# Performance work log

Hardware: AMD Instinct MI355X
Metric: run time of the kernel (lower is better)

Reference implementation:

```python
import jax, jax.numpy as jnp
import numpy as np

N, E = 50000, 800000          # nodes, directed edges (before self-loops)
IN, H, C = 128, 8, 32         # in_feats, heads, per-head channels (= h_feats)
G = 64                        # graphs in batch
NEG_SLOPE = 0.2               # PyG GATConv default leaky_relu slope


def setup_inputs() -> dict:
    key = jax.random.key(0)
    ks = jax.random.split(key, 8)
    x = jax.random.normal(ks[0], (N, IN), jnp.float32)
    edge_index = jax.random.randint(ks[1], (2, E), 0, N)
    batch = jnp.sort(jax.random.randint(ks[2], (N,), 0, G))
    W = jax.random.normal(ks[3], (IN, H * C), jnp.float32) * 0.05
    att_src = jax.random.normal(ks[4], (H, C), jnp.float32) * 0.1
    att_dst = jax.random.normal(ks[5], (H, C), jnp.float32) * 0.1
    bias = jnp.zeros((C,), jnp.float32)
    lin_w = jax.random.normal(ks[6], (C, 2), jnp.float32) * 0.1
    lin_b = jnp.zeros((2,), jnp.float32)
    return dict(x=x, edge_index=edge_index, batch=batch, W=W,
                att_src=att_src, att_dst=att_dst, bias=bias,
                lin_w=lin_w, lin_b=lin_b)


def gat_conv(x, edge_index, W, att_src, att_dst, bias):
    # PyG GATConv, heads=H, concat=False, add_self_loops=True
    n = x.shape[0]
    h = (x @ W).reshape(n, H, C)                      # [N,H,C]
    loops = jnp.arange(n, dtype=edge_index.dtype)
    src = jnp.concatenate([edge_index[0], loops])     # [E+N]
    dst = jnp.concatenate([edge_index[1], loops])
    a_src = jnp.einsum('nhc,hc->nh', h, att_src)      # [N,H]
    a_dst = jnp.einsum('nhc,hc->nh', h, att_dst)
    e = jax.nn.leaky_relu(a_src[src] + a_dst[dst], NEG_SLOPE)  # [E+N,H]
    # segment softmax over edges sharing the same destination node
    m = jax.ops.segment_max(e, dst, num_segments=n)
    m = jnp.where(jnp.isfinite(m), m, 0.0)            # guard isolated nodes
    w = jnp.exp(e - m[dst])
    denom = jax.ops.segment_sum(w, dst, num_segments=n)
    alpha = w / (denom[dst] + 1e-16)                  # [E+N,H]
    out = jax.ops.segment_sum(h[src] * alpha[:, :, None], dst, num_segments=n)  # [N,H,C]
    return out.mean(axis=1) + bias                    # concat=False -> head mean


def reference(x, edge_index, batch, W, att_src, att_dst, bias, lin_w, lin_b):
    hid = jax.nn.relu(gat_conv(x, edge_index, W, att_src, att_dst, bias))  # [N,C]
    sums = jax.ops.segment_sum(hid, batch, num_segments=G)                  # [G,C]
    cnt = jax.ops.segment_sum(jnp.ones((hid.shape[0],), hid.dtype), batch,
                              num_segments=G)
    pooled = sums / jnp.maximum(cnt, 1.0)[:, None]    # global_mean_pool
    # Dropout(0.5) is identity in eval mode
    x_t = pooled @ lin_w + lin_b                      # [G,2]
    return (x_t, pooled)
```

## Files before the change

### kernel.cpp

```cpp
#include <hip/hip_runtime.h>
#include <hip/hip_bf16.h>

#define N_NODES 50000
#define E_EDGES 800000
#define IN_F 128
#define H_HEADS 8
#define C_CH 32
#define HC 256
#define G_GRAPHS 64
#define NEG_SLOPE 0.2f
#define NCHUNK 49

__device__ __forceinline__ unsigned short f2bf(float f) {
    unsigned u = __float_as_uint(f);
    u += 0x7fffu + ((u >> 16) & 1u);
    return (unsigned short)(u >> 16);
}

__global__ __launch_bounds__(256) void k_gemm(const float* __restrict__ x,
        const float* __restrict__ W, const float* __restrict__ att_src,
        const float* __restrict__ att_dst, unsigned short* __restrict__ hb,
        float* __restrict__ a_src, float* __restrict__ a_dst) {
    __shared__ float xs[8 * IN_F];
    const int n0 = blockIdx.x * 8;
    const int tid = threadIdx.x;
    ((float4*)xs)[tid] = ((const float4*)(x + (size_t)n0 * IN_F))[tid];
    __syncthreads();

    const int j = tid;
    float acc[8];
    #pragma unroll
    for (int r = 0; r < 8; ++r) acc[r] = 0.f;

    const float4* xs4 = (const float4*)xs;
    for (int k4 = 0; k4 < IN_F / 4; ++k4) {
        const float w0 = W[(k4 * 4 + 0) * HC + j];
        const float w1 = W[(k4 * 4 + 1) * HC + j];
        const float w2 = W[(k4 * 4 + 2) * HC + j];
        const float w3 = W[(k4 * 4 + 3) * HC + j];
        #pragma unroll
        for (int r = 0; r < 8; ++r) {
            float4 xv = xs4[r * (IN_F / 4) + k4];
            acc[r] += xv.x * w0 + xv.y * w1 + xv.z * w2 + xv.w * w3;
        }
    }

    const float asv = att_src[j], adv = att_dst[j];
    const int hh = j >> 5;
    #pragma unroll
    for (int r = 0; r < 8; ++r) {
        hb[(size_t)(n0 + r) * HC + j] = f2bf(acc[r]);
        float s = acc[r] * asv, d = acc[r] * adv;
        #pragma unroll
        for (int off = 16; off; off >>= 1) {
            s += __shfl_xor(s, off, 64);
            d += __shfl_xor(d, off, 64);
        }
        if ((tid & 31) == 0) {
            a_src[(n0 + r) * H_HEADS + hh] = s;
            a_dst[(n0 + r) * H_HEADS + hh] = d;
        }
    }
}

__global__ __launch_bounds__(256) void k_hist(const int* __restrict__ ei,
        int* __restrict__ deg) {
    int i = blockIdx.x * 256 + threadIdx.x;
    if (i < E_EDGES) atomicAdd(deg + ei[E_EDGES + i], 1);
}

__global__ __launch_bounds__(256) void k_chunksum(const int* __restrict__ deg,
        int* __restrict__ chunk) {
    __shared__ int ws4[4];
    const int tid = threadIdx.x, lane = tid & 63, wid = tid >> 6;
    const int base = blockIdx.x * 1024 + tid * 4;
    int s = 0;
    #pragma unroll
    for (int u = 0; u < 4; ++u) {
        int i = base + u;
        if (i < N_NODES) s += deg[i];
    }
    #pragma unroll
    for (int o = 32; o; o >>= 1) s += __shfl_xor(s, o, 64);
    if (lane == 0) ws4[wid] = s;
    __syncthreads();
    if (tid == 0) chunk[blockIdx.x] = ws4[0] + ws4[1] + ws4[2] + ws4[3];
}

__global__ __launch_bounds__(64) void k_chunkscan(const int* __restrict__ chunk,
        int* __restrict__ chunkoff) {
    int t = threadIdx.x;
    int v = (t < NCHUNK) ? chunk[t] : 0;
    int s = v;
    #pragma unroll
    for (int d = 1; d < 64; d <<= 1) {
        int u = __shfl_up(s, d, 64);
        if (t >= d) s += u;
    }
    if (t < NCHUNK) chunkoff[t] = s - v;
}

__global__ __launch_bounds__(1024) void k_localscan(const int* __restrict__ deg,
        const int* __restrict__ chunkoff, int* __restrict__ off,
        int* __restrict__ cursor) {
    __shared__ int wsum[16];
    const int tid = threadIdx.x, lane = tid & 63, wid = tid >> 6;
    const int i = blockIdx.x * 1024 + tid;
    int v = (i < N_NODES) ? deg[i] : 0;
    int s = v;
    #pragma unroll
    for (int d = 1; d < 64; d <<= 1) {
        int t = __shfl_up(s, d, 64);
        if (lane >= d) s += t;
    }
    if (lane == 63) wsum[wid] = s;
    __syncthreads();
    if (wid == 0 && lane < 16) {
        int t = wsum[lane];
        #pragma unroll
        for (int d = 1; d < 16; d <<= 1) {
            int u = __shfl_up(t, d, 64);
            if (lane >= d) t += u;
        }
        wsum[lane] = t;
    }
    __syncthreads();
    int wpre = wid ? wsum[wid - 1] : 0;
    if (i < N_NODES) {
        int excl = chunkoff[blockIdx.x] + wpre + s - v;
        off[i] = excl;
        cursor[i] = excl;
    }
    if (blockIdx.x == NCHUNK - 1 && tid == 0) off[N_NODES] = E_EDGES;
}

__global__ __launch_bounds__(256) void k_scatter(const int* __restrict__ ei,
        int* __restrict__ cursor, int* __restrict__ csr_src) {
    int i = blockIdx.x * 256 + threadIdx.x;
    if (i >= E_EDGES) return;
    int dst = ei[E_EDGES + i];
    int p = atomicAdd(cursor + dst, 1);
    csr_src[p] = ei[i];
}

__device__ __forceinline__ void bf4_unpack(uint2 q, float& x0, float& x1,
                                           float& x2, float& x3) {
    x0 = __uint_as_float(q.x << 16);
    x1 = __uint_as_float(q.x & 0xffff0000u);
    x2 = __uint_as_float(q.y << 16);
    x3 = __uint_as_float(q.y & 0xffff0000u);
}

__global__ __launch_bounds__(256) void k_node(const unsigned short* __restrict__ hb,
        const float* __restrict__ a_src, const float* __restrict__ a_dst,
        const int* __restrict__ off, const int* __restrict__ csr_src,
        const int* __restrict__ batch, const float* __restrict__ bias,
        float* __restrict__ pool, float* __restrict__ cnt) {
    const int wave = threadIdx.x >> 6, lane = threadIdx.x & 63;
    const int n = blockIdx.x * 4 + wave;
    if (n >= N_NODES) return;
    const int hh = lane >> 3;
    const int beg = off[n], end = off[n + 1];
    const float adst = a_dst[n * H_HEADS + hh];

    float denom = 0.f;
    float ax = 0.f, ay = 0.f, az = 0.f, aw = 0.f;
    {
        float e = a_src[n * H_HEADS + hh] + adst;
        e = e > 0.f ? e : NEG_SLOPE * e;
        float w = __expf(e);
        denom += w;
        uint2 q = ((const uint2*)(hb + (size_t)n * HC))[lane];
        float x0, x1, x2, x3; bf4_unpack(q, x0, x1, x2, x3);
        ax += w * x0; ay += w * x1; az += w * x2; aw += w * x3;
    }

    int k = beg;
    for (; k + 7 < end; k += 8) {
        int s[8];
        #pragma unroll
        for (int u = 0; u < 8; ++u) s[u] = csr_src[k + u];
        uint2 q[8];
        #pragma unroll
        for (int u = 0; u < 8; ++u)
            q[u] = ((const uint2*)(hb + (size_t)s[u] * HC))[lane];
        float e[8];
        #pragma unroll
        for (int u = 0; u < 8; ++u) e[u] = a_src[s[u] * H_HEADS + hh] + adst;
        #pragma unroll
        for (int u = 0; u < 8; ++u) {
            float ee = e[u] > 0.f ? e[u] : NEG_SLOPE * e[u];
            float w = __expf(ee);
            denom += w;
            float x0, x1, x2, x3; bf4_unpack(q[u], x0, x1, x2, x3);
            ax += w * x0; ay += w * x1; az += w * x2; aw += w * x3;
        }
    }
    for (; k < end; ++k) {
        int src = csr_src[k];
        float e = a_src[src * H_HEADS + hh] + adst;
        e = e > 0.f ? e : NEG_SLOPE * e;
        float w = __expf(e);
        denom += w;
        uint2 q = ((const uint2*)(hb + (size_t)src * HC))[lane];
        float x0, x1, x2, x3; bf4_unpack(q, x0, x1, x2, x3);
        ax += w * x0; ay += w * x1; az += w * x2; aw += w * x3;
    }

    const float inv = 1.f / (denom + 1e-16f);
    float rx = ax * inv, ry = ay * inv, rz = az * inv, rw = aw * inv;
    #pragma unroll
    for (int o = 8; o < 64; o <<= 1) {
        rx += __shfl_xor(rx, o, 64);
        ry += __shfl_xor(ry, o, 64);
        rz += __shfl_xor(rz, o, 64);
        rw += __shfl_xor(rw, o, 64);
    }
    if (lane < 8) {
        const int c0 = lane * 4;
        const int g = batch[n];
        float o0 = fmaxf(rx * 0.125f + bias[c0 + 0], 0.f);
        float o1 = fmaxf(ry * 0.125f + bias[c0 + 1], 0.f);
        float o2 = fmaxf(rz * 0.125f + bias[c0 + 2], 0.f);
        float o3 = fmaxf(rw * 0.125f + bias[c0 + 3], 0.f);
        float* pg = pool + g * C_CH + c0;
        atomicAdd(pg + 0, o0); atomicAdd(pg + 1, o1);
        atomicAdd(pg + 2, o2); atomicAdd(pg + 3, o3);
        if (lane == 0) atomicAdd(cnt + g, 1.f);
    }
}

__global__ __launch_bounds__(256) void k_final(const float* __restrict__ pool,
        const float* __restrict__ cnt, const float* __restrict__ lin_w,
        const float* __restrict__ lin_b, float* __restrict__ out) {
    __shared__ float pd[G_GRAPHS * C_CH];
    int t = threadIdx.x;
    for (int i = t; i < G_GRAPHS * C_CH; i += 256) {
        int g = i >> 5;
        float p = pool[i] / fmaxf(cnt[g], 1.f);
        pd[i] = p;
        out[G_GRAPHS * 2 + i] = p;
    }
    __syncthreads();
    if (t < G_GRAPHS * 2) {
        int g = t >> 1, o = t & 1;
        float s = lin_b[o];
        #pragma unroll
        for (int c = 0; c < C_CH; ++c) s += pd[g * C_CH + c] * lin_w[c * 2 + o];
        out[t] = s;
    }
}

extern "C" void kernel_launch(void* const* d_in, const int* in_sizes, int n_in,
                              void* d_out, int out_size, void* d_ws, size_t ws_size,
                              hipStream_t stream) {
    const float* x       = (const float*)d_in[0];
    const int*   ei      = (const int*)d_in[1];
    const int*   batch   = (const int*)d_in[2];
    const float* W       = (const float*)d_in[3];
    const float* att_src = (const float*)d_in[4];
    const float* att_dst = (const float*)d_in[5];
    const float* bias    = (const float*)d_in[6];
    const float* lin_w   = (const float*)d_in[7];
    const float* lin_b   = (const float*)d_in[8];

    char* ws = (char*)d_ws;
    unsigned short* hb   = (unsigned short*)(ws);
    float* a_src   = (float*)(ws + 25600000);
    float* a_dst   = (float*)(ws + 27200000);
    int*   deg     = (int*)  (ws + 28800000);
    int*   chunk   = (int*)  (ws + 29000000);
    int*   off     = (int*)  (ws + 29000256);
    int*   cursor  = (int*)  (ws + 29200512);
    int*   csr_src = (int*)  (ws + 29400512);
    float* pool    = (float*)(ws + 32600512);
    float* cnt     = (float*)(ws + 32608704);
    int*   chunkoff= (int*)  (ws + 32608960);

    hipMemsetAsync(deg, 0, 200000, stream);
    hipMemsetAsync(pool, 0, 8192 + 256, stream);

    k_gemm<<<N_NODES / 8, 256, 0, stream>>>(x, W, att_src, att_dst, hb, a_src, a_dst);
    k_hist<<<(E_EDGES + 255) / 256, 256, 0, stream>>>(ei, deg);
    k_chunksum<<<NCHUNK, 256, 0, stream>>>(deg, chunk);
    k_chunkscan<<<1, 64, 0, stream>>>(chunk, chunkoff);
    k_localscan<<<NCHUNK, 1024, 0, stream>>>(deg, chunkoff, off, cursor);
    k_scatter<<<(E_EDGES + 255) / 256, 256, 0, stream>>>(ei, cursor, csr_src);
    k_node<<<(N_NODES + 3) / 4, 256, 0, stream>>>(
        hb, a_src, a_dst, off, csr_src, batch, bias, pool, cnt);
    k_final<<<1, 256, 0, stream>>>(pool, cnt, lin_w, lin_b, (float*)d_out);
}
```

Before: 730.9 us.

## Process two edges per wave with 16-byte gathers and software-pipelined loads

The node aggregation kernel now splits each 64-lane wave into two halves. Each half handles a different edge and loads a 512-byte bf16 row with uint4 (16-byte) loads instead of uint2. The main loop double-buffers batches of four gathers so the next batch's loads are in flight while the current one is accumulated. The halves are merged with a cross-half shuffle, and the reduction across heads and the pooling atomics are adjusted to 8 channels per lane. The aim is wider memory transactions and more memory-level parallelism, at the cost of more registers and some extra odd-count tail handling.

```diff
diff --git a/kernel.cpp b/kernel.cpp
--- a/kernel.cpp
+++ b/kernel.cpp
@@ -143,12 +143,15 @@
     csr_src[p] = ei[i];
 }
 
-__device__ __forceinline__ void bf4_unpack(uint2 q, float& x0, float& x1,
-                                           float& x2, float& x3) {
-    x0 = __uint_as_float(q.x << 16);
-    x1 = __uint_as_float(q.x & 0xffff0000u);
-    x2 = __uint_as_float(q.y << 16);
-    x3 = __uint_as_float(q.y & 0xffff0000u);
+__device__ __forceinline__ void accum8w(float* acc, uint4 q, float w) {
+    acc[0] += w * __uint_as_float(q.x << 16);
+    acc[1] += w * __uint_as_float(q.x & 0xffff0000u);
+    acc[2] += w * __uint_as_float(q.y << 16);
+    acc[3] += w * __uint_as_float(q.y & 0xffff0000u);
+    acc[4] += w * __uint_as_float(q.z << 16);
+    acc[5] += w * __uint_as_float(q.z & 0xffff0000u);
+    acc[6] += w * __uint_as_float(q.w << 16);
+    acc[7] += w * __uint_as_float(q.w & 0xffff0000u);
 }
 
 __global__ __launch_bounds__(256) void k_node(const unsigned short* __restrict__ hb,
@@ -159,73 +162,102 @@
     const int wave = threadIdx.x >> 6, lane = threadIdx.x & 63;
     const int n = blockIdx.x * 4 + wave;
     if (n >= N_NODES) return;
-    const int hh = lane >> 3;
+    const int half = lane >> 5;
+    const int l32 = lane & 31;
+    const int hh = l32 >> 2;
     const int beg = off[n], end = off[n + 1];
     const float adst = a_dst[n * H_HEADS + hh];
 
+    float acc[8] = {0.f, 0.f, 0.f, 0.f, 0.f, 0.f, 0.f, 0.f};
     float denom = 0.f;
-    float ax = 0.f, ay = 0.f, az = 0.f, aw = 0.f;
+
     {
         float e = a_src[n * H_HEADS + hh] + adst;
         e = e > 0.f ? e : NEG_SLOPE * e;
-        float w = __expf(e);
+        float w = half ? 0.f : __expf(e);
+        uint4 q = ((const uint4*)(hb + (size_t)n * HC))[l32];
         denom += w;
-        uint2 q = ((const uint2*)(hb + (size_t)n * HC))[lane];
-        float x0, x1, x2, x3; bf4_unpack(q, x0, x1, x2, x3);
-        ax += w * x0; ay += w * x1; az += w * x2; aw += w * x3;
-    }
-
-    int k = beg;
-    for (; k + 7 < end; k += 8) {
-        int s[8];
-        #pragma unroll
-        for (int u = 0; u < 8; ++u) s[u] = csr_src[k + u];
-        uint2 q[8];
-        #pragma unroll
-        for (int u = 0; u < 8; ++u)
-            q[u] = ((const uint2*)(hb + (size_t)s[u] * HC))[lane];
-        float e[8];
-        #pragma unroll
-        for (int u = 0; u < 8; ++u) e[u] = a_src[s[u] * H_HEADS + hh] + adst;
-        #pragma unroll
-        for (int u = 0; u < 8; ++u) {
-            float ee = e[u] > 0.f ? e[u] : NEG_SLOPE * e[u];
-            float w = __expf(ee);
+        accum8w(acc, q, w);
+    }
+
+    auto issue = [&](int kk, uint4* q, float* ea) {
+        #pragma unroll
+        for (int u = 0; u < 4; ++u) {
+            int s0 = csr_src[kk + 2 * u];
+            int s1 = csr_src[kk + 2 * u + 1];
+            int s = half ? s1 : s0;
+            q[u] = ((const uint4*)(hb + (size_t)s * HC))[l32];
+            ea[u] = a_src[s * H_HEADS + hh];
+        }
+    };
+    auto consume = [&](const uint4* q, const float* ea) {
+        #pragma unroll
+        for (int u = 0; u < 4; ++u) {
+            float e = ea[u] + adst;
+            e = e > 0.f ? e : NEG_SLOPE * e;
+            float w = __expf(e);
             denom += w;
-            float x0, x1, x2, x3; bf4_unpack(q[u], x0, x1, x2, x3);
-            ax += w * x0; ay += w * x1; az += w * x2; aw += w * x3;
-        }
-    }
-    for (; k < end; ++k) {
-        int src = csr_src[k];
-        float e = a_src[src * H_HEADS + hh] + adst;
+            accum8w(acc, q[u], w);
+        }
+    };
+
+    const int nfull = (end - beg) & ~7;
+    const int nb = nfull >> 3;
+    uint4 qA[4], qB[4];
+    float eA[4], eB[4];
+    if (nb > 0) {
+        issue(beg, qA, eA);
+        for (int b = 1; b < nb; ++b) {
+            if (b & 1) { issue(beg + 8 * b, qB, eB); consume(qA, eA); }
+            else       { issue(beg + 8 * b, qA, eA); consume(qB, eB); }
+        }
+        if (nb & 1) consume(qA, eA); else consume(qB, eB);
+    }
+
+    int k = beg + nfull;
+    for (; k + 1 < end; k += 2) {
+        int s0 = csr_src[k], s1 = csr_src[k + 1];
+        int s = half ? s1 : s0;
+        uint4 q = ((const uint4*)(hb + (size_t)s * HC))[l32];
+        float e = a_src[s * H_HEADS + hh] + adst;
         e = e > 0.f ? e : NEG_SLOPE * e;
         float w = __expf(e);
         denom += w;
-        uint2 q = ((const uint2*)(hb + (size_t)src * HC))[lane];
-        float x0, x1, x2, x3; bf4_unpack(q, x0, x1, x2, x3);
-        ax += w * x0; ay += w * x1; az += w * x2; aw += w * x3;
-    }
-
-    const float inv = 1.f / (denom + 1e-16f);
-    float rx = ax * inv, ry = ay * inv, rz = az * inv, rw = aw * inv;
-    #pragma unroll
-    for (int o = 8; o < 64; o <<= 1) {
-        rx += __shfl_xor(rx, o, 64);
-        ry += __shfl_xor(ry, o, 64);
-        rz += __shfl_xor(rz, o, 64);
-        rw += __shfl_xor(rw, o, 64);
-    }
-    if (lane < 8) {
-        const int c0 = lane * 4;
+        accum8w(acc, q, w);
+    }
+    if (k < end) {
+        int s = csr_src[k];
+        uint4 q = ((const uint4*)(hb + (size_t)s * HC))[l32];
+        float e = a_src[s * H_HEADS + hh] + adst;
+        e = e > 0.f ? e : NEG_SLOPE * e;
+        float w = half ? 0.f : __expf(e);
+        denom += w;
+        accum8w(acc, q, w);
+    }
+
+    #pragma unroll
+    for (int j = 0; j < 8; ++j) acc[j] += __shfl_xor(acc[j], 32, 64);
+    denom += __shfl_xor(denom, 32, 64);
+
+    const float inv = 0.125f / (denom + 1e-16f);
+    float r[8];
+    #pragma unroll
+    for (int j = 0; j < 8; ++j) r[j] = acc[j] * inv;
+    #pragma unroll
+    for (int o = 4; o <= 16; o <<= 1) {
+        #pragma unroll
+        for (int j = 0; j < 8; ++j) r[j] += __shfl_xor(r[j], o, 64);
+    }
+    if (lane < 4) {
         const int g = batch[n];
-        float o0 = fmaxf(rx * 0.125f + bias[c0 + 0], 0.f);
-        float o1 = fmaxf(ry * 0.125f + bias[c0 + 1], 0.f);
-        float o2 = fmaxf(rz * 0.125f + bias[c0 + 2], 0.f);
-        float o3 = fmaxf(rw * 0.125f + bias[c0 + 3], 0.f);
+        const int c0 = lane * 8;
         float* pg = pool + g * C_CH + c0;
-        atomicAdd(pg + 0, o0); atomicAdd(pg + 1, o1);
-        atomicAdd(pg + 2, o2); atomicAdd(pg + 3, o3);
+        #pragma unroll
+        for (int j = 0; j < 8; ++j) {
+            float o = r[j] + bias[c0 + j];
+            o = o > 0.f ? o : 0.f;
+            atomicAdd(pg + j, o);
+        }
         if (lane == 0) atomicAdd(cnt + g, 1.f);
     }
 }
```

Result: slower. 778.6 us (+6.5%).

## Switch node-parallel aggregation to edge-parallel with segmented atomic accumulation

Applied to the files above, without the earlier changes.

Replaces the per-destination-node wave loop with an edge-parallel kernel. Each wave handles 8 consecutive CSR-sorted edges, merges runs that share a destination, and atomically adds the weighted features and denominators into a float accumulator of size N×256. A self-loop kernel initialises the accumulator and a finalize kernel normalises, averages heads, applies ReLU and pools. This aims to remove load imbalance from varying in-degrees, at the cost of writing and reading a large fp32 accumulator, many float atomics, and an extra csr_dst array.

```diff
diff --git a/kernel.cpp b/kernel.cpp
--- a/kernel.cpp
+++ b/kernel.cpp
@@ -101,8 +101,7 @@
 }
 
 __global__ __launch_bounds__(1024) void k_localscan(const int* __restrict__ deg,
-        const int* __restrict__ chunkoff, int* __restrict__ off,
-        int* __restrict__ cursor) {
+        const int* __restrict__ chunkoff, int* __restrict__ cursor) {
     __shared__ int wsum[16];
     const int tid = threadIdx.x, lane = tid & 63, wid = tid >> 6;
     const int i = blockIdx.x * 1024 + tid;
@@ -126,21 +125,18 @@
     }
     __syncthreads();
     int wpre = wid ? wsum[wid - 1] : 0;
-    if (i < N_NODES) {
-        int excl = chunkoff[blockIdx.x] + wpre + s - v;
-        off[i] = excl;
-        cursor[i] = excl;
-    }
-    if (blockIdx.x == NCHUNK - 1 && tid == 0) off[N_NODES] = E_EDGES;
+    if (i < N_NODES) cursor[i] = chunkoff[blockIdx.x] + wpre + s - v;
 }
 
 __global__ __launch_bounds__(256) void k_scatter(const int* __restrict__ ei,
-        int* __restrict__ cursor, int* __restrict__ csr_src) {
+        int* __restrict__ cursor, int* __restrict__ csr_src,
+        int* __restrict__ csr_dst) {
     int i = blockIdx.x * 256 + threadIdx.x;
     if (i >= E_EDGES) return;
     int dst = ei[E_EDGES + i];
     int p = atomicAdd(cursor + dst, 1);
     csr_src[p] = ei[i];
+    csr_dst[p] = dst;
 }
 
 __device__ __forceinline__ void bf4_unpack(uint2 q, float& x0, float& x1,
@@ -151,83 +147,83 @@
     x3 = __uint_as_float(q.y & 0xffff0000u);
 }
 
-__global__ __launch_bounds__(256) void k_node(const unsigned short* __restrict__ hb,
+__global__ __launch_bounds__(256) void k_selfloop(const unsigned short* __restrict__ hb,
         const float* __restrict__ a_src, const float* __restrict__ a_dst,
-        const int* __restrict__ off, const int* __restrict__ csr_src,
-        const int* __restrict__ batch, const float* __restrict__ bias,
-        float* __restrict__ pool, float* __restrict__ cnt) {
+        float* __restrict__ outacc, float* __restrict__ den) {
     const int wave = threadIdx.x >> 6, lane = threadIdx.x & 63;
     const int n = blockIdx.x * 4 + wave;
     if (n >= N_NODES) return;
     const int hh = lane >> 3;
-    const int beg = off[n], end = off[n + 1];
-    const float adst = a_dst[n * H_HEADS + hh];
-
-    float denom = 0.f;
-    float ax = 0.f, ay = 0.f, az = 0.f, aw = 0.f;
-    {
-        float e = a_src[n * H_HEADS + hh] + adst;
+    float e = a_src[n * H_HEADS + hh] + a_dst[n * H_HEADS + hh];
+    e = e > 0.f ? e : NEG_SLOPE * e;
+    float w = __expf(e);
+    uint2 q = ((const uint2*)(hb + (size_t)n * HC))[lane];
+    float x0, x1, x2, x3; bf4_unpack(q, x0, x1, x2, x3);
+    float* oa = outacc + (size_t)n * HC + lane * 4;
+    oa[0] = w * x0; oa[1] = w * x1; oa[2] = w * x2; oa[3] = w * x3;
+    if ((lane & 7) == 0) den[n * H_HEADS + hh] = w;
+}
+
+__global__ __launch_bounds__(256) void k_edge(const unsigned short* __restrict__ hb,
+        const float* __restrict__ a_src, const float* __restrict__ a_dst,
+        const int* __restrict__ csr_src, const int* __restrict__ csr_dst,
+        float* __restrict__ outacc, float* __restrict__ den) {
+    const int wid = blockIdx.x * 4 + (threadIdx.x >> 6);
+    const int lane = threadIdx.x & 63;
+    const int kb = wid * 8;
+    if (kb >= E_EDGES) return;
+    const int hh = lane >> 3;
+
+    int s[8], d[8];
+    #pragma unroll
+    for (int u = 0; u < 8; ++u) { s[u] = csr_src[kb + u]; d[u] = csr_dst[kb + u]; }
+    uint2 q[8];
+    #pragma unroll
+    for (int u = 0; u < 8; ++u)
+        q[u] = ((const uint2*)(hb + (size_t)s[u] * HC))[lane];
+    float w[8];
+    #pragma unroll
+    for (int u = 0; u < 8; ++u) {
+        float e = a_src[s[u] * H_HEADS + hh] + a_dst[d[u] * H_HEADS + hh];
         e = e > 0.f ? e : NEG_SLOPE * e;
-        float w = __expf(e);
-        denom += w;
-        uint2 q = ((const uint2*)(hb + (size_t)n * HC))[lane];
-        float x0, x1, x2, x3; bf4_unpack(q, x0, x1, x2, x3);
-        ax += w * x0; ay += w * x1; az += w * x2; aw += w * x3;
-    }
-
-    int k = beg;
-    for (; k + 7 < end; k += 8) {
-        int s[8];
-        #pragma unroll
-        for (int u = 0; u < 8; ++u) s[u] = csr_src[k + u];
-        uint2 q[8];
-        #pragma unroll
-        for (int u = 0; u < 8; ++u)
-            q[u] = ((const uint2*)(hb + (size_t)s[u] * HC))[lane];
-        float e[8];
-        #pragma unroll
-        for (int u = 0; u < 8; ++u) e[u] = a_src[s[u] * H_HEADS + hh] + adst;
-        #pragma unroll
-        for (int u = 0; u < 8; ++u) {
-            float ee = e[u] > 0.f ? e[u] : NEG_SLOPE * e[u];
-            float w = __expf(ee);
-            denom += w;
-            float x0, x1, x2, x3; bf4_unpack(q[u], x0, x1, x2, x3);
-            ax += w * x0; ay += w * x1; az += w * x2; aw += w * x3;
-        }
-    }
-    for (; k < end; ++k) {
-        int src = csr_src[k];
-        float e = a_src[src * H_HEADS + hh] + adst;
-        e = e > 0.f ? e : NEG_SLOPE * e;
-        float w = __expf(e);
-        denom += w;
-        uint2 q = ((const uint2*)(hb + (size_t)src * HC))[lane];
-        float x0, x1, x2, x3; bf4_unpack(q, x0, x1, x2, x3);
-        ax += w * x0; ay += w * x1; az += w * x2; aw += w * x3;
-    }
-
-    const float inv = 1.f / (denom + 1e-16f);
-    float rx = ax * inv, ry = ay * inv, rz = az * inv, rw = aw * inv;
-    #pragma unroll
-    for (int o = 8; o < 64; o <<= 1) {
-        rx += __shfl_xor(rx, o, 64);
-        ry += __shfl_xor(ry, o, 64);
-        rz += __shfl_xor(rz, o, 64);
-        rw += __shfl_xor(rw, o, 64);
-    }
-    if (lane < 8) {
-        const int c0 = lane * 4;
-        const int g = batch[n];
-        float o0 = fmaxf(rx * 0.125f + bias[c0 + 0], 0.f);
-        float o1 = fmaxf(ry * 0.125f + bias[c0 + 1], 0.f);
-        float o2 = fmaxf(rz * 0.125f + bias[c0 + 2], 0.f);
-        float o3 = fmaxf(rw * 0.125f + bias[c0 + 3], 0.f);
-        float* pg = pool + g * C_CH + c0;
-        atomicAdd(pg + 0, o0); atomicAdd(pg + 1, o1);
-        atomicAdd(pg + 2, o2); atomicAdd(pg + 3, o3);
-        if (lane == 0) atomicAdd(cnt + g, 1.f);
-    }
+        w[u] = __expf(e);
+    }
+
+    float a0 = 0.f, a1 = 0.f, a2 = 0.f, a3 = 0.f, dn = 0.f;
+    #pragma unroll
+    for (int u = 0; u < 8; ++u) {
+        float x0, x1, x2, x3; bf4_unpack(q[u], x0, x1, x2, x3);
+        a0 += w[u] * x0; a1 += w[u] * x1;
+        a2 += w[u] * x2; a3 += w[u] * x3;
+        dn += w[u];
+        bool fl = (u == 7) ? true : (d[u + 1] != d[u]);
+        if (fl) {
+            float* oa = outacc + (size_t)d[u] * HC + lane * 4;
+            atomicAdd(oa + 0, a0); atomicAdd(oa + 1, a1);
+            atomicAdd(oa + 2, a2); atomicAdd(oa + 3, a3);
+            if ((lane & 7) == 0) atomicAdd(den + d[u] * H_HEADS + hh, dn);
+            a0 = a1 = a2 = a3 = dn = 0.f;
+        }
+    }
+}
+
+__global__ __launch_bounds__(256) void k_finalize(const float* __restrict__ outacc,
+        const float* __restrict__ den, const float* __restrict__ bias,
+        const int* __restrict__ batch, float* __restrict__ pool,
+        float* __restrict__ cnt) {
+    int idx = blockIdx.x * 256 + threadIdx.x;
+    if (idx >= N_NODES * C_CH) return;
+    int n = idx >> 5, c = idx & 31;
+    float s = 0.f;
+    #pragma unroll
+    for (int hh = 0; hh < H_HEADS; ++hh)
+        s += outacc[(size_t)n * HC + hh * C_CH + c]
+             / (den[n * H_HEADS + hh] + 1e-16f);
+    s = s * 0.125f + bias[c];
+    s = s > 0.f ? s : 0.f;
+    int g = batch[n];
+    atomicAdd(pool + g * C_CH + c, s);
+    if (c == 0) atomicAdd(cnt + g, 1.f);
 }
 
 __global__ __launch_bounds__(256) void k_final(const float* __restrict__ pool,
@@ -270,12 +266,14 @@
     float* a_dst   = (float*)(ws + 27200000);
     int*   deg     = (int*)  (ws + 28800000);
     int*   chunk   = (int*)  (ws + 29000000);
-    int*   off     = (int*)  (ws + 29000256);
-    int*   cursor  = (int*)  (ws + 29200512);
-    int*   csr_src = (int*)  (ws + 29400512);
-    float* pool    = (float*)(ws + 32600512);
-    float* cnt     = (float*)(ws + 32608704);
-    int*   chunkoff= (int*)  (ws + 32608960);
+    int*   cursor  = (int*)  (ws + 29000256);
+    int*   csr_src = (int*)  (ws + 29200256);
+    int*   csr_dst = (int*)  (ws + 32400256);
+    float* pool    = (float*)(ws + 35600256);
+    float* cnt     = (float*)(ws + 35608448);
+    int*   chunkoff= (int*)  (ws + 35608704);
+    float* outacc  = (float*)(ws + 35608960);
+    float* den     = (float*)(ws + 86808960);
 
     hipMemsetAsync(deg, 0, 200000, stream);
     hipMemsetAsync(pool, 0, 8192 + 256, stream);
@@ -284,9 +282,12 @@
     k_hist<<<(E_EDGES + 255) / 256, 256, 0, stream>>>(ei, deg);
     k_chunksum<<<NCHUNK, 256, 0, stream>>>(deg, chunk);
     k_chunkscan<<<1, 64, 0, stream>>>(chunk, chunkoff);
-    k_localscan<<<NCHUNK, 1024, 0, stream>>>(deg, chunkoff, off, cursor);
-    k_scatter<<<(E_EDGES + 255) / 256, 256, 0, stream>>>(ei, cursor, csr_src);
-    k_node<<<(N_NODES + 3) / 4, 256, 0, stream>>>(
-        hb, a_src, a_dst, off, csr_src, batch, bias, pool, cnt);
+    k_localscan<<<NCHUNK, 1024, 0, stream>>>(deg, chunkoff, cursor);
+    k_scatter<<<(E_EDGES + 255) / 256, 256, 0, stream>>>(ei, cursor, csr_src, csr_dst);
+    k_selfloop<<<(N_NODES + 3) / 4, 256, 0, stream>>>(hb, a_src, a_dst, outacc, den);
+    k_edge<<<(E_EDGES / 8 + 3) / 4, 256, 0, stream>>>(
+        hb, a_src, a_dst, csr_src, csr_dst, outacc, den);
+    k_finalize<<<(N_NODES * C_CH + 255) / 256, 256, 0, stream>>>(
+        outacc, den, bias, batch, pool, cnt);
     k_final<<<1, 256, 0, stream>>>(pool, cnt, lin_w, lin_b, (float*)d_out);
 }
```

New measurement: 1.168 ms. 1.6x slower.
